# Performance work log

Hardware: AMD Instinct MI355X
Metric: run time of the kernel (lower is better)

The kernel has to match this reference:

```python
import jax, jax.numpy as jnp
import numpy as np

EMBED_DIM = 1024
B, S = 4, 2048

def setup_inputs() -> dict:
    key = jax.random.key(0)
    ks = jax.random.split(key, 9)
    D = EMBED_DIM
    scale = 1.0 / np.sqrt(D)
    scale2 = 1.0 / np.sqrt(2 * D)
    return {
        "classical_state": jax.random.normal(ks[0], (B, S, D), jnp.float32),
        "quantum_state": jax.random.normal(ks[1], (B, S, D), jnp.float32),
        "Wc": jax.random.uniform(ks[2], (D, D), jnp.float32, -scale, scale),
        "bc": jax.random.uniform(ks[3], (D,), jnp.float32, -scale, scale),
        "Wq": jax.random.uniform(ks[4], (D, D), jnp.float32, -scale, scale),
        "bq": jax.random.uniform(ks[5], (D,), jnp.float32, -scale, scale),
        "Wg": jax.random.uniform(ks[6], (D, 2 * D), jnp.float32, -scale2, scale2),
        "bg": jax.random.uniform(ks[7], (D,), jnp.float32, -scale2, scale2),
        "temperature": jnp.array(1.0, jnp.float32),
    }

def reference(classical_state, quantum_state, Wc, bc, Wq, bq, Wg, bg, temperature):
    D = classical_state.shape[-1]
    c_proj = jnp.einsum('bsd,ed->bse', classical_state, Wc) + bc  # [B,S,D]
    q_proj = jnp.einsum('bsd,ed->bse', quantum_state, Wq) + bq    # [B,S,D]
    combined = jnp.concatenate([c_proj, q_proj], axis=-1)         # [B,S,2D]
    interface_state = jax.nn.sigmoid(jnp.einsum('bsf,ef->bse', combined, Wg) + bg)
    similarity = jnp.einsum('bsd,btd->bst', c_proj, q_proj) / jnp.sqrt(jnp.asarray(D, c_proj.dtype))
    attention_weights = jax.nn.softmax(similarity / temperature, axis=-1)  # [B,S,S]
    transfer_state = jnp.einsum('bst,btd->bsd', attention_weights, quantum_state)
    return classical_state + interface_state * transfer_state
```

## Files before the change

kernel.cpp:

```cpp
#include <hip/hip_runtime.h>


typedef unsigned short u16;
typedef unsigned char u8;
typedef __bf16 bf16x8 __attribute__((ext_vector_type(8)));
typedef float f32x4 __attribute__((ext_vector_type(4)));
typedef int i32x4 __attribute__((ext_vector_type(4)));
typedef int i32x8 __attribute__((ext_vector_type(8)));
typedef short short8 __attribute__((ext_vector_type(8)));

__device__ __forceinline__ u16 f2bf(float f) {
    unsigned int x;
    __builtin_memcpy(&x, &f, 4);
    unsigned int r = x + 0x7FFFu + ((x >> 16) & 1u);
    return (u16)(r >> 16);
}
__device__ __forceinline__ float bf2f(u16 u) {
    unsigned int x = ((unsigned int)u) << 16;
    float f;
    __builtin_memcpy(&f, &x, 4);
    return f;
}
__device__ __forceinline__ u8 f2fp8(float f) {
    int p = __builtin_amdgcn_cvt_pk_fp8_f32(f, f, 0, false);
    return (u8)(p & 0xFF);
}

__device__ __forceinline__ void xcd_tile(int& tx, int& ty) {
    const int gx = gridDim.x;
    const int nwg = gx * gridDim.y;
    const int l = blockIdx.x + gx * blockIdx.y;
    const int per = nwg >> 3;
    const int swz = (l & 7) * per + (l >> 3);
    tx = swz % gx;
    ty = swz / gx;
}

#define GLOBAL_TO_LDS16(gp, lp)                                                           \
    __builtin_amdgcn_global_load_lds((const __attribute__((address_space(1))) void*)(gp), \
                                     (__attribute__((address_space(3))) void*)(lp), 16, 0, 0)

__global__ __launch_bounds__(256, 2) void gemm_proj(
    const u16* __restrict__ Ac, const u16* __restrict__ Aq, int lda,
    const u16* __restrict__ Bp, long sBz, int ldb,
    u8* __restrict__ C8, long sCz, int ldc, int K,
    const float* __restrict__ bc, const float* __restrict__ bq) {
    __shared__ __align__(16) u16 As[2][128 * 64];
    __shared__ __align__(16) u16 Bs[2][128 * 64];

    const int tid  = threadIdx.x;
    const int lane = tid & 63;
    const int wave = tid >> 6;
    const int z    = blockIdx.z;

    const u16* a = z ? Aq : Ac;
    const u16* b = Bp + (long)z * sBz;
    const float* bias = z ? bq : bc;

    int tx, ty;
    xcd_tile(tx, ty);
    const int tileM = ty * 128;
    const int tileN = tx * 128;

    const int wm  = wave >> 1;
    const int wn  = wave & 1;
    const int r16 = lane & 15;
    const int kg  = lane >> 4;

    const int srow = lane >> 3;
    const int sgc  = ((lane & 7) ^ (lane >> 3)) * 8;
    const int swb  = r16 & 7;

    auto stage = [&](int buf, int t) {
        const int k0 = t * 64;
#pragma unroll
        for (int p = 0; p < 4; p++) {
            const int rbase = p * 32 + wave * 8;
            GLOBAL_TO_LDS16(a + (long)(tileM + rbase + srow) * lda + k0 + sgc, &As[buf][rbase * 64]);
            GLOBAL_TO_LDS16(b + (long)(tileN + rbase + srow) * ldb + k0 + sgc, &Bs[buf][rbase * 64]);
        }
    };

    f32x4 acc[4][4] = {};

    const int nt = K / 64;
    stage(0, 0);
    stage(1, 1);

    for (int t = 0; t < nt; t++) {
        const int cur = t & 1;
        if (t + 1 < nt) asm volatile("s_waitcnt vmcnt(8)" ::: "memory");
        else            asm volatile("s_waitcnt vmcnt(0)" ::: "memory");
        __builtin_amdgcn_s_barrier();
        asm volatile("" ::: "memory");

        bf16x8 af[2][4], bfr[2][4];
#pragma unroll
        for (int h = 0; h < 2; h++) {
#pragma unroll
            for (int i = 0; i < 4; i++) {
                const int Ra = wm * 64 + i * 16 + r16;
                af[h][i]  = *(const bf16x8*)&As[cur][Ra * 64 + (((h * 4 + kg) ^ swb)) * 8];
                const int Rb = wn * 64 + i * 16 + r16;
                bfr[h][i] = *(const bf16x8*)&Bs[cur][Rb * 64 + (((h * 4 + kg) ^ swb)) * 8];
            }
        }
#pragma unroll
        for (int h = 0; h < 2; h++)
#pragma unroll
            for (int i = 0; i < 4; i++)
#pragma unroll
                for (int j = 0; j < 4; j++)
                    acc[i][j] = __builtin_amdgcn_mfma_f32_16x16x32_bf16(
                        af[h][i], bfr[h][j], acc[i][j], 0, 0, 0);

        asm volatile("" ::: "memory");
        __builtin_amdgcn_s_barrier();
        if (t + 2 < nt) stage(cur, t + 2);
    }

#pragma unroll
    for (int i = 0; i < 4; i++)
#pragma unroll
        for (int j = 0; j < 4; j++) {
            int col = tileN + wn * 64 + j * 16 + r16;
            float bv = bias[col];
#pragma unroll
            for (int v = 0; v < 4; v++) {
                int row = tileM + wm * 64 + i * 16 + kg * 4 + v;
                C8[(long)z * sCz + (long)row * ldc + col] = f2fp8(acc[i][j][v] + bv);
            }
        }
}

template <int MODE>
__global__ __launch_bounds__(256, 2) void gemm8(
    const u8* __restrict__ A0, const u8* __restrict__ A1, long sAz, int lda, int kSplit,
    const u8* __restrict__ Bp, long sBz, int ldb,
    void* __restrict__ Cp, long cOff, long sCz, int ldc, int K,
    const float* __restrict__ bias, const float* __restrict__ temp,
    const float* __restrict__ cls, const u16* __restrict__ g16,
    float* __restrict__ lsum, long lSz) {
    __shared__ __align__(16) u8 As[128 * 128];
    __shared__ __align__(16) u8 Bs[128 * 128];

    const int tid  = threadIdx.x;
    const int lane = tid & 63;
    const int wave = tid >> 6;
    const int z    = blockIdx.z;

    const u8* a = A0 + (long)z * sAz;
    const u8* b = Bp + (long)z * sBz;

    int tx, ty;
    xcd_tile(tx, ty);
    const int tileM = ty * 128;
    const int tileN = tx * 128;

    const int wm  = wave >> 1;
    const int wn  = wave & 1;
    const int r16 = lane & 15;
    const int kg  = lane >> 4;

    const int srow = lane >> 3;
    const int sgc  = ((lane & 7) ^ (lane >> 3)) * 16;

    f32x4 acc[4][4] = {};

    for (int k0 = 0; k0 < K; k0 += 128) {
        const u8* Ap = a;
        int kA = k0;
        if (MODE == 1 && k0 >= kSplit) { Ap = A1; kA = k0 - kSplit; }

#pragma unroll
        for (int p = 0; p < 4; p++) {
            const int rbase = p * 32 + wave * 8;
            GLOBAL_TO_LDS16(Ap + (long)(tileM + rbase + srow) * lda + kA + sgc, &As[rbase * 128]);
            GLOBAL_TO_LDS16(b + (long)(tileN + rbase + srow) * ldb + k0 + sgc, &Bs[rbase * 128]);
        }
        __syncthreads();

        i32x8 af[4];
#pragma unroll
        for (int i = 0; i < 4; i++) {
            const int Ra = wm * 64 + i * 16 + r16;
            const u8* base = &As[Ra * 128];
            *(i32x4*)&af[i]       = *(const i32x4*)&base[(((2 * kg)     ^ (Ra & 7))) * 16];
            *((i32x4*)&af[i] + 1) = *(const i32x4*)&base[(((2 * kg + 1) ^ (Ra & 7))) * 16];
        }
#pragma unroll
        for (int j = 0; j < 4; j++) {
            const int Rb = wn * 64 + j * 16 + r16;
            const u8* base = &Bs[Rb * 128];
            i32x8 bfr;
            *(i32x4*)&bfr       = *(const i32x4*)&base[(((2 * kg)     ^ (Rb & 7))) * 16];
            *((i32x4*)&bfr + 1) = *(const i32x4*)&base[(((2 * kg + 1) ^ (Rb & 7))) * 16];
#pragma unroll
            for (int i = 0; i < 4; i++)
                acc[i][j] = __builtin_amdgcn_mfma_scale_f32_16x16x128_f8f6f4(
                    af[i], bfr, acc[i][j], 0, 0, 0, 127, 0, 127);
        }
        __syncthreads();
    }

    u16*   C16 = (u16*)Cp;
    u8*    C8  = (u8*)Cp;
    float* C32 = (float*)Cp;

    if constexpr (MODE == 2) {
        const float scale = 1.0f / (32.0f * temp[0]);
        u8* Cs = As;
#pragma unroll
        for (int i = 0; i < 4; i++) {
            float rs[4] = {0.f, 0.f, 0.f, 0.f};
#pragma unroll
            for (int j = 0; j < 4; j++) {
                const int lcol = wn * 64 + j * 16 + r16;
#pragma unroll
                for (int v = 0; v < 4; v++) {
                    const int lrow = wm * 64 + i * 16 + kg * 4 + v;
                    float e = __expf(acc[i][j][v] * scale);
                    Cs[lrow * 128 + (lcol ^ ((lrow & 12) << 2))] = f2fp8(e);
                    rs[v] += e;
                }
            }
#pragma unroll
            for (int v = 0; v < 4; v++) {
                float s = rs[v];
#pragma unroll
                for (int off = 1; off < 16; off <<= 1) s += __shfl_xor(s, off, 64);
                if (r16 == 0) {
                    int row = tileM + wm * 64 + i * 16 + kg * 4 + v;
                    atomicAdd(&lsum[(long)z * lSz + row], s);
                }
            }
        }
        __syncthreads();
        const int r  = tid >> 1;
        const int ch = (tid & 1) * 64;
        const int rk = (r >> 2) & 3;
        i32x4 w[4];
#pragma unroll
        for (int m = 0; m < 4; m++)
            w[m] = *(const i32x4*)&Cs[r * 128 + ch + ((m ^ rk) << 4)];
        long base = cOff + (long)z * sCz + (long)(tileM + r) * ldc + tileN + ch;
#pragma unroll
        for (int m = 0; m < 4; m++)
            *(i32x4*)&C8[base + m * 16] = w[m];
    } else {
#pragma unroll
        for (int i = 0; i < 4; i++) {
#pragma unroll
            for (int j = 0; j < 4; j++) {
                int col = tileN + wn * 64 + j * 16 + r16;
                float bv = (MODE == 1) ? bias[col] : 0.0f;
#pragma unroll
                for (int v = 0; v < 4; v++) {
                    int row = tileM + wm * 64 + i * 16 + kg * 4 + v;
                    long idx = cOff + (long)z * sCz + (long)row * ldc + col;
                    float val = acc[i][j][v];
                    if (MODE == 1) {
                        C16[idx] = f2bf(1.0f / (1.0f + __expf(-(val + bv))));
                    } else {
                        float inv = 1.0f / lsum[(long)z * lSz + row];
                        C32[idx] = cls[idx] + bf2f(g16[idx]) * (val * inv);
                    }
                }
            }
        }
    }
}

__global__ __launch_bounds__(256) void prep(
    const f32x4* __restrict__ cls, const f32x4* __restrict__ qnt,
    const f32x4* __restrict__ Wc, const f32x4* __restrict__ Wq, const f32x4* __restrict__ Wg,
    ushort4* __restrict__ clsB, ushort4* __restrict__ qntB,
    ushort4* __restrict__ WcB, ushort4* __restrict__ WqB, unsigned int* __restrict__ Wg8,
    f32x4* __restrict__ l, long nM, long nW, long nG, long nL) {
    long i = (long)blockIdx.x * 256 + threadIdx.x;
    long stride = (long)gridDim.x * 256;
    long total = 2 * nM + 2 * nW + nG + nL;
    for (; i < total; i += stride) {
        if (i < 2 * nM) {
            long j = (i < nM) ? i : i - nM;
            f32x4 v = (i < nM) ? cls[j] : qnt[j];
            ushort4 o;
            o.x = f2bf(v.x); o.y = f2bf(v.y); o.z = f2bf(v.z); o.w = f2bf(v.w);
            if (i < nM) clsB[j] = o; else qntB[j] = o;
        } else if (i < 2 * nM + 2 * nW) {
            long j = i - 2 * nM;
            long k = (j < nW) ? j : j - nW;
            f32x4 v = (j < nW) ? Wc[k] : Wq[k];
            ushort4 o;
            o.x = f2bf(v.x); o.y = f2bf(v.y); o.z = f2bf(v.z); o.w = f2bf(v.w);
            if (j < nW) WcB[k] = o; else WqB[k] = o;
        } else if (i < 2 * nM + 2 * nW + nG) {
            long j = i - 2 * nM - 2 * nW;
            f32x4 v = Wg[j];
            int w = __builtin_amdgcn_cvt_pk_fp8_f32(v.x, v.y, 0, false);
            w = __builtin_amdgcn_cvt_pk_fp8_f32(v.z, v.w, w, true);
            Wg8[j] = (unsigned int)w;
        } else {
            l[i - 2 * nM - 2 * nW - nG] = (f32x4){0.f, 0.f, 0.f, 0.f};
        }
    }
}

__global__ __launch_bounds__(256) void transpose_fp8(const u16* __restrict__ Q,
                                                     u8* __restrict__ QT, int S, int D) {
    __shared__ __align__(16) u8 tile[64][80];
    int bz = blockIdx.z;
    const u16* q = Q + (long)bz * S * D;
    u8* qt = QT + (long)bz * S * D;
    int t0 = blockIdx.x * 64;
    int d0 = blockIdx.y * 64;
    {
        const int r  = threadIdx.x >> 2;
        const int dc = (threadIdx.x & 3) * 16;
        const u16* src = q + (long)(t0 + r) * D + d0 + dc;
        short8 a = *(const short8*)src;
        short8 bqv = *(const short8*)(src + 8);
        unsigned int pk[4];
#pragma unroll
        for (int m = 0; m < 2; m++) {
            int w = __builtin_amdgcn_cvt_pk_fp8_f32(
                bf2f((u16)a[4 * m + 0]), bf2f((u16)a[4 * m + 1]), 0, false);
            w = __builtin_amdgcn_cvt_pk_fp8_f32(
                bf2f((u16)a[4 * m + 2]), bf2f((u16)a[4 * m + 3]), w, true);
            pk[m] = (unsigned int)w;
        }
#pragma unroll
        for (int m = 0; m < 2; m++) {
            int w = __builtin_amdgcn_cvt_pk_fp8_f32(
                bf2f((u16)bqv[4 * m + 0]), bf2f((u16)bqv[4 * m + 1]), 0, false);
            w = __builtin_amdgcn_cvt_pk_fp8_f32(
                bf2f((u16)bqv[4 * m + 2]), bf2f((u16)bqv[4 * m + 3]), w, true);
            pk[2 + m] = (unsigned int)w;
        }
        *(i32x4*)&tile[r][dc] = *(i32x4*)pk;
    }
    __syncthreads();
    {
        const int dl = threadIdx.x >> 2;
        const int tc = (threadIdx.x & 3) * 16;
        unsigned int w[4];
#pragma unroll
        for (int m = 0; m < 4; m++) {
            unsigned int x = 0;
#pragma unroll
            for (int k = 0; k < 4; k++)
                x |= (unsigned int)tile[tc + m * 4 + k][dl] << (8 * k);
            w[m] = x;
        }
        *(i32x4*)&qt[(long)(d0 + dl) * S + t0 + tc] = *(i32x4*)w;
    }
}

extern "C" void kernel_launch(void* const* d_in, const int* in_sizes, int n_in,
                              void* d_out, int out_size, void* d_ws, size_t ws_size,
                              hipStream_t stream) {
    (void)in_sizes; (void)n_in; (void)out_size;

    const float* classical = (const float*)d_in[0];
    const float* quantum   = (const float*)d_in[1];
    const float* Wc        = (const float*)d_in[2];
    const float* bc        = (const float*)d_in[3];
    const float* Wq        = (const float*)d_in[4];
    const float* bq        = (const float*)d_in[5];
    const float* Wg        = (const float*)d_in[6];
    const float* bg        = (const float*)d_in[7];
    const float* temp      = (const float*)d_in[8];
    float* out = (float*)d_out;

    const int B = 4, S = 2048, D = 1024;
    const long MD = (long)B * S * D;

    float* l    = (float*)d_ws;
    u16* Wc_b   = (u16*)(l + (long)B * S);
    u16* Wq_b   = Wc_b + (long)D * D;
    u8*  Wg8    = (u8*)(Wq_b + (long)D * D);
    u16* cls_b  = (u16*)(Wg8 + (long)D * 2 * D);
    u16* qnt_b  = cls_b + MD;
    u8*  cp8    = (u8*)(qnt_b + MD);
    u8*  qp8    = cp8 + MD;
    u8*  qT8    = qp8 + MD;
    u8*  P8     = qT8 + MD;
    u16* g      = cls_b;

    const size_t fixed_bytes = (size_t)B * S * 4 + 2 * (size_t)D * D * 2 +
        (size_t)D * 2 * D + 2 * (size_t)MD * 2 + 3 * (size_t)MD;
    int CH = 128;
    for (int c = 2048; c >= 128; c >>= 1) {
        if (ws_size >= fixed_bytes + (size_t)B * c * S) { CH = c; break; }
    }

    dim3 blk(256);

    prep<<<2048, blk, 0, stream>>>(
        (const f32x4*)classical, (const f32x4*)quantum,
        (const f32x4*)Wc, (const f32x4*)Wq, (const f32x4*)Wg,
        (ushort4*)cls_b, (ushort4*)qnt_b,
        (ushort4*)Wc_b, (ushort4*)Wq_b, (unsigned int*)Wg8,
        (f32x4*)l, MD / 4, (long)D * D / 4, (long)D * 2 * D / 4, (long)B * S / 4);

    gemm_proj<<<dim3(D / 128, (B * S) / 128, 2), blk, 0, stream>>>(
        cls_b, qnt_b, D, Wc_b, (long)D * D, D, cp8, MD, D, D, bc, bq);

    gemm8<1><<<dim3(D / 128, (B * S) / 128, 1), blk, 0, stream>>>(
        cp8, qp8, 0, D, D, Wg8, 0, 2 * D, g, 0, 0, D, 2 * D,
        bg, nullptr, nullptr, nullptr, nullptr, 0);

    transpose_fp8<<<dim3(S / 64, D / 64, B), blk, 0, stream>>>(qnt_b, qT8, S, D);

    for (int m0 = 0; m0 < S; m0 += CH) {
        gemm8<2><<<dim3(S / 128, CH / 128, B), blk, 0, stream>>>(
            cp8 + (long)m0 * D, nullptr, (long)S * D, D, 1 << 30,
            qp8, (long)S * D, D, P8, 0, (long)CH * S, S, D,
            nullptr, temp, nullptr, nullptr, l + m0, S);
        gemm8<4><<<dim3(D / 128, CH / 128, B), blk, 0, stream>>>(
            P8, nullptr, (long)CH * S, S, 1 << 30, qT8, (long)D * S, S,
            out, (long)m0 * D, (long)S * D, D, S,
            nullptr, nullptr, classical, g, l + m0, S);
    }
}
```

Measured before the change: 267.0 us.

## Fuse gate GEMM with first similarity chunk and transpose into prep kernel

```diff
diff --git a/kernel.cpp b/kernel.cpp
--- a/kernel.cpp
+++ b/kernel.cpp
@@ -134,28 +134,20 @@
 }
 
 template <int MODE>
-__global__ __launch_bounds__(256, 2) void gemm8(
+__device__ __forceinline__ void gemm8_body(
+    int tileM, int tileN, int z, int tid,
     const u8* __restrict__ A0, const u8* __restrict__ A1, long sAz, int lda, int kSplit,
     const u8* __restrict__ Bp, long sBz, int ldb,
     void* __restrict__ Cp, long cOff, long sCz, int ldc, int K,
     const float* __restrict__ bias, const float* __restrict__ temp,
     const float* __restrict__ cls, const u16* __restrict__ g16,
-    float* __restrict__ lsum, long lSz) {
-    __shared__ __align__(16) u8 As[128 * 128];
-    __shared__ __align__(16) u8 Bs[128 * 128];
-
-    const int tid  = threadIdx.x;
+    float* __restrict__ lsum, long lSz,
+    u8* As, u8* Bs) {
     const int lane = tid & 63;
     const int wave = tid >> 6;
-    const int z    = blockIdx.z;
 
     const u8* a = A0 + (long)z * sAz;
     const u8* b = Bp + (long)z * sBz;
-
-    int tx, ty;
-    xcd_tile(tx, ty);
-    const int tileM = ty * 128;
-    const int tileN = tx * 128;
 
     const int wm  = wave >> 1;
     const int wn  = wave & 1;
@@ -271,88 +263,127 @@
     }
 }
 
-__global__ __launch_bounds__(256) void prep(
+template <int MODE>
+__global__ __launch_bounds__(256, 2) void gemm8(
+    const u8* __restrict__ A0, const u8* __restrict__ A1, long sAz, int lda, int kSplit,
+    const u8* __restrict__ Bp, long sBz, int ldb,
+    void* __restrict__ Cp, long cOff, long sCz, int ldc, int K,
+    const float* __restrict__ bias, const float* __restrict__ temp,
+    const float* __restrict__ cls, const u16* __restrict__ g16,
+    float* __restrict__ lsum, long lSz) {
+    __shared__ __align__(16) u8 As[128 * 128];
+    __shared__ __align__(16) u8 Bs[128 * 128];
+    int tx, ty;
+    xcd_tile(tx, ty);
+    gemm8_body<MODE>(ty * 128, tx * 128, blockIdx.z, threadIdx.x,
+                     A0, A1, sAz, lda, kSplit, Bp, sBz, ldb,
+                     Cp, cOff, sCz, ldc, K, bias, temp, cls, g16, lsum, lSz, As, Bs);
+}
+
+__global__ __launch_bounds__(256, 2) void gateSim(
+    const u8* __restrict__ cp8, const u8* __restrict__ qp8,
+    const u8* __restrict__ Wg8, u16* __restrict__ g, const float* __restrict__ bg,
+    u8* __restrict__ P8, long sP, const float* __restrict__ temp,
+    float* __restrict__ lsum, long lSz,
+    long sBD, int D, int S, int nwgSim) {
+    __shared__ __align__(16) u8 As[128 * 128];
+    __shared__ __align__(16) u8 Bs[128 * 128];
+    const int bid = blockIdx.x;
+    if (bid < 512) {
+        const int swz = (bid & 7) * 64 + (bid >> 3);
+        const int tx = swz & 7, ty = swz >> 3;
+        gemm8_body<1>(ty * 128, tx * 128, 0, threadIdx.x,
+                      cp8, qp8, 0, D, D, Wg8, 0, 2 * D,
+                      g, 0, 0, D, 2 * D,
+                      bg, nullptr, nullptr, nullptr, nullptr, 0, As, Bs);
+    } else {
+        const int sb  = bid - 512;
+        const int z   = sb / nwgSim;
+        const int lid = sb - z * nwgSim;
+        const int per = nwgSim >> 3;
+        const int swz = (lid & 7) * per + (lid >> 3);
+        const int tx = swz & 15, ty = swz >> 4;
+        gemm8_body<2>(ty * 128, tx * 128, z, threadIdx.x,
+                      cp8, nullptr, sBD, D, 1 << 30, qp8, sBD, D,
+                      P8, 0, sP, S, D,
+                      nullptr, temp, nullptr, nullptr, lsum, lSz, As, Bs);
+    }
+}
+
+__global__ __launch_bounds__(256) void prepT(
     const f32x4* __restrict__ cls, const f32x4* __restrict__ qnt,
     const f32x4* __restrict__ Wc, const f32x4* __restrict__ Wq, const f32x4* __restrict__ Wg,
     ushort4* __restrict__ clsB, ushort4* __restrict__ qntB,
     ushort4* __restrict__ WcB, ushort4* __restrict__ WqB, unsigned int* __restrict__ Wg8,
-    f32x4* __restrict__ l, long nM, long nW, long nG, long nL) {
-    long i = (long)blockIdx.x * 256 + threadIdx.x;
-    long stride = (long)gridDim.x * 256;
-    long total = 2 * nM + 2 * nW + nG + nL;
-    for (; i < total; i += stride) {
-        if (i < 2 * nM) {
-            long j = (i < nM) ? i : i - nM;
-            f32x4 v = (i < nM) ? cls[j] : qnt[j];
-            ushort4 o;
-            o.x = f2bf(v.x); o.y = f2bf(v.y); o.z = f2bf(v.z); o.w = f2bf(v.w);
-            if (i < nM) clsB[j] = o; else qntB[j] = o;
-        } else if (i < 2 * nM + 2 * nW) {
-            long j = i - 2 * nM;
-            long k = (j < nW) ? j : j - nW;
-            f32x4 v = (j < nW) ? Wc[k] : Wq[k];
-            ushort4 o;
-            o.x = f2bf(v.x); o.y = f2bf(v.y); o.z = f2bf(v.z); o.w = f2bf(v.w);
-            if (j < nW) WcB[k] = o; else WqB[k] = o;
-        } else if (i < 2 * nM + 2 * nW + nG) {
-            long j = i - 2 * nM - 2 * nW;
-            f32x4 v = Wg[j];
-            int w = __builtin_amdgcn_cvt_pk_fp8_f32(v.x, v.y, 0, false);
-            w = __builtin_amdgcn_cvt_pk_fp8_f32(v.z, v.w, w, true);
-            Wg8[j] = (unsigned int)w;
-        } else {
-            l[i - 2 * nM - 2 * nW - nG] = (f32x4){0.f, 0.f, 0.f, 0.f};
-        }
-    }
-}
-
-__global__ __launch_bounds__(256) void transpose_fp8(const u16* __restrict__ Q,
-                                                     u8* __restrict__ QT, int S, int D) {
+    f32x4* __restrict__ l, long nM, long nW, long nG, long nL,
+    const float* __restrict__ Qf, u8* __restrict__ QT, int S, int D) {
     __shared__ __align__(16) u8 tile[64][80];
-    int bz = blockIdx.z;
-    const u16* q = Q + (long)bz * S * D;
-    u8* qt = QT + (long)bz * S * D;
-    int t0 = blockIdx.x * 64;
-    int d0 = blockIdx.y * 64;
-    {
-        const int r  = threadIdx.x >> 2;
-        const int dc = (threadIdx.x & 3) * 16;
-        const u16* src = q + (long)(t0 + r) * D + d0 + dc;
-        short8 a = *(const short8*)src;
-        short8 bqv = *(const short8*)(src + 8);
-        unsigned int pk[4];
-#pragma unroll
-        for (int m = 0; m < 2; m++) {
-            int w = __builtin_amdgcn_cvt_pk_fp8_f32(
-                bf2f((u16)a[4 * m + 0]), bf2f((u16)a[4 * m + 1]), 0, false);
-            w = __builtin_amdgcn_cvt_pk_fp8_f32(
-                bf2f((u16)a[4 * m + 2]), bf2f((u16)a[4 * m + 3]), w, true);
-            pk[m] = (unsigned int)w;
-        }
-#pragma unroll
-        for (int m = 0; m < 2; m++) {
-            int w = __builtin_amdgcn_cvt_pk_fp8_f32(
-                bf2f((u16)bqv[4 * m + 0]), bf2f((u16)bqv[4 * m + 1]), 0, false);
-            w = __builtin_amdgcn_cvt_pk_fp8_f32(
-                bf2f((u16)bqv[4 * m + 2]), bf2f((u16)bqv[4 * m + 3]), w, true);
-            pk[2 + m] = (unsigned int)w;
-        }
-        *(i32x4*)&tile[r][dc] = *(i32x4*)pk;
-    }
-    __syncthreads();
-    {
-        const int dl = threadIdx.x >> 2;
-        const int tc = (threadIdx.x & 3) * 16;
-        unsigned int w[4];
-#pragma unroll
-        for (int m = 0; m < 4; m++) {
-            unsigned int x = 0;
-#pragma unroll
-            for (int k = 0; k < 4; k++)
-                x |= (unsigned int)tile[tc + m * 4 + k][dl] << (8 * k);
-            w[m] = x;
-        }
-        *(i32x4*)&qt[(long)(d0 + dl) * S + t0 + tc] = *(i32x4*)w;
+    const int bid = blockIdx.x;
+    if (bid < 2048) {
+        long i = (long)bid * 256 + threadIdx.x;
+        const long stride = 2048L * 256;
+        const long total = 2 * nM + 2 * nW + nG + nL;
+        for (; i < total; i += stride) {
+            if (i < 2 * nM) {
+                long j = (i < nM) ? i : i - nM;
+                f32x4 v = (i < nM) ? cls[j] : qnt[j];
+                ushort4 o;
+                o.x = f2bf(v.x); o.y = f2bf(v.y); o.z = f2bf(v.z); o.w = f2bf(v.w);
+                if (i < nM) clsB[j] = o; else qntB[j] = o;
+            } else if (i < 2 * nM + 2 * nW) {
+                long j = i - 2 * nM;
+                long k = (j < nW) ? j : j - nW;
+                f32x4 v = (j < nW) ? Wc[k] : Wq[k];
+                ushort4 o;
+                o.x = f2bf(v.x); o.y = f2bf(v.y); o.z = f2bf(v.z); o.w = f2bf(v.w);
+                if (j < nW) WcB[k] = o; else WqB[k] = o;
+            } else if (i < 2 * nM + 2 * nW + nG) {
+                long j = i - 2 * nM - 2 * nW;
+                f32x4 v = Wg[j];
+                int w = __builtin_amdgcn_cvt_pk_fp8_f32(v.x, v.y, 0, false);
+                w = __builtin_amdgcn_cvt_pk_fp8_f32(v.z, v.w, w, true);
+                Wg8[j] = (unsigned int)w;
+            } else {
+                l[i - 2 * nM - 2 * nW - nG] = (f32x4){0.f, 0.f, 0.f, 0.f};
+            }
+        }
+    } else {
+        const int tb = bid - 2048;
+        const int bx = tb & 31;
+        const int by = (tb >> 5) & 15;
+        const int bz = tb >> 9;
+        const float* q = Qf + (long)bz * S * D;
+        u8* qt = QT + (long)bz * S * D;
+        const int t0 = bx * 64, d0 = by * 64;
+        {
+            const int r  = threadIdx.x >> 2;
+            const int dc = (threadIdx.x & 3) * 16;
+            const float* src = q + (long)(t0 + r) * D + d0 + dc;
+            unsigned int pk[4];
+#pragma unroll
+            for (int m = 0; m < 4; m++) {
+                f32x4 v = *(const f32x4*)(src + 4 * m);
+                int w = __builtin_amdgcn_cvt_pk_fp8_f32(v.x, v.y, 0, false);
+                w = __builtin_amdgcn_cvt_pk_fp8_f32(v.z, v.w, w, true);
+                pk[m] = (unsigned int)w;
+            }
+            *(i32x4*)&tile[r][dc] = *(i32x4*)pk;
+        }
+        __syncthreads();
+        {
+            const int dl = threadIdx.x >> 2;
+            const int tc = (threadIdx.x & 3) * 16;
+            unsigned int w[4];
+#pragma unroll
+            for (int m = 0; m < 4; m++) {
+                unsigned int x = 0;
+#pragma unroll
+                for (int k = 0; k < 4; k++)
+                    x |= (unsigned int)tile[tc + m * 4 + k][dl] << (8 * k);
+                w[m] = x;
+            }
+            *(i32x4*)&qt[(long)(d0 + dl) * S + t0 + tc] = *(i32x4*)w;
+        }
     }
 }
 
@@ -393,31 +424,38 @@
     for (int c = 2048; c >= 128; c >>= 1) {
         if (ws_size >= fixed_bytes + (size_t)B * c * S) { CH = c; break; }
     }
+    const int chDiv  = CH / 128;
+    const int nwgSim = (S / 128) * chDiv;
 
     dim3 blk(256);
 
-    prep<<<2048, blk, 0, stream>>>(
+    prepT<<<4096, blk, 0, stream>>>(
         (const f32x4*)classical, (const f32x4*)quantum,
         (const f32x4*)Wc, (const f32x4*)Wq, (const f32x4*)Wg,
         (ushort4*)cls_b, (ushort4*)qnt_b,
         (ushort4*)Wc_b, (ushort4*)Wq_b, (unsigned int*)Wg8,
-        (f32x4*)l, MD / 4, (long)D * D / 4, (long)D * 2 * D / 4, (long)B * S / 4);
+        (f32x4*)l, MD / 4, (long)D * D / 4, (long)D * 2 * D / 4, (long)B * S / 4,
+        quantum, qT8, S, D);
 
     gemm_proj<<<dim3(D / 128, (B * S) / 128, 2), blk, 0, stream>>>(
         cls_b, qnt_b, D, Wc_b, (long)D * D, D, cp8, MD, D, D, bc, bq);
 
-    gemm8<1><<<dim3(D / 128, (B * S) / 128, 1), blk, 0, stream>>>(
-        cp8, qp8, 0, D, D, Wg8, 0, 2 * D, g, 0, 0, D, 2 * D,
-        bg, nullptr, nullptr, nullptr, nullptr, 0);
-
-    transpose_fp8<<<dim3(S / 64, D / 64, B), blk, 0, stream>>>(qnt_b, qT8, S, D);
-
-    for (int m0 = 0; m0 < S; m0 += CH) {
-        gemm8<2><<<dim3(S / 128, CH / 128, B), blk, 0, stream>>>(
+    gateSim<<<512 + B * nwgSim, blk, 0, stream>>>(
+        cp8, qp8, Wg8, g, bg,
+        P8, (long)CH * S, temp, l, S,
+        (long)S * D, D, S, nwgSim);
+
+    gemm8<4><<<dim3(D / 128, chDiv, B), blk, 0, stream>>>(
+        P8, nullptr, (long)CH * S, S, 1 << 30, qT8, (long)D * S, S,
+        out, 0, (long)S * D, D, S,
+        nullptr, nullptr, classical, g, l, S);
+
+    for (int m0 = CH; m0 < S; m0 += CH) {
+        gemm8<2><<<dim3(S / 128, chDiv, B), blk, 0, stream>>>(
             cp8 + (long)m0 * D, nullptr, (long)S * D, D, 1 << 30,
             qp8, (long)S * D, D, P8, 0, (long)CH * S, S, D,
             nullptr, temp, nullptr, nullptr, l + m0, S);
-        gemm8<4><<<dim3(D / 128, CH / 128, B), blk, 0, stream>>>(
+        gemm8<4><<<dim3(D / 128, chDiv, B), blk, 0, stream>>>(
             P8, nullptr, (long)CH * S, S, 1 << 30, qT8, (long)D * S, S,
             out, (long)m0 * D, (long)S * D, D, S,
             nullptr, nullptr, classical, g, l + m0, S);
```

Result: faster. 247.7 us (-7.3%).
